# Optimization experiments

Measured on AMD Instinct MI355X. Metric: run time of the kernel, lower is better.

Reference implementation:

```python
import jax, jax.numpy as jnp
import numpy as np
from jax import lax

C_OUT, C_IN, KH, KW = 16, 16, 3, 3
STRIDE = (1, 1)
PADDING = ((1, 1), (1, 1))  # symmetric 'same' padding for 3x3, stride 1
DILATION = (1, 1)


def setup_inputs() -> dict:
    key = jax.random.key(0)
    kx, kw = jax.random.split(key)
    x = jax.random.normal(kx, (8, C_IN, 512, 512), dtype=jnp.float32)
    # Conv2DUF stores the conv weight flattened: [out_channels, in_channels*kh*kw]
    weight = jax.random.normal(kw, (C_OUT, C_IN * KH * KW), dtype=jnp.float32) * 0.1
    return {"x": x, "weight": weight}


def reference(x, weight):
    # forward(): F.conv2d(x, weight.reshape(original shape), stride/padding/dilation/groups)
    w = weight.reshape(C_OUT, C_IN, KH, KW)
    out = lax.conv_general_dilated(
        x, w,
        window_strides=STRIDE,
        padding=PADDING,
        rhs_dilation=DILATION,
        dimension_numbers=("NCHW", "OIHW", "NCHW"),
        feature_group_count=1,
    )
    return out  # [8, 16, 512, 512]
```

## Files before the change

### kernel.cpp

```cpp
#include <hip/hip_runtime.h>
#include <hip/hip_bf16.h>


#define IH 512
#define IW 512
#define CI 16
#define CO 16
#define TH 16
#define TW 32
#define LROWS (TH + 2)
#define LCOLS (TW + 2)
#define NITEMS (LROWS * (TW / 4) * 4)

typedef short short8  __attribute__((ext_vector_type(8)));
typedef short short4v __attribute__((ext_vector_type(4)));
typedef float f32x4   __attribute__((ext_vector_type(4)));

__device__ __forceinline__ short f32_to_bf16_bits(float v) {
    __hip_bfloat16 b = __float2bfloat16(v);
    return __builtin_bit_cast(short, b);
}

struct ItemInfo {
    const float* src;
    int pb;
    int ws;
    int cg;
    bool ok;
};

__device__ __forceinline__ ItemInfo item_info(int i, int hbase, int wbase,
                                              const float* __restrict__ xn) {
    ItemInfo t;
    t.ws = i & 7;
    t.cg = (i >> 3) & 3;
    const int row = i >> 5;
    const int gh  = hbase - 1 + row;
    t.ok  = (unsigned)gh < (unsigned)IH;
    t.src = xn + ((size_t)(t.cg * 4) * IH + gh) * IW + (wbase + 4 * t.ws);
    t.pb  = row * LCOLS + 1 + 4 * t.ws;
    return t;
}

__device__ __forceinline__ void item_load(const ItemInfo& t, f32x4 v[4]) {
    if (t.ok) {
#pragma unroll
        for (int jj = 0; jj < 4; ++jj)
            v[jj] = *(const f32x4*)(t.src + (size_t)jj * IH * IW);
    }
}

__device__ __forceinline__ void item_store(const ItemInfo& t, const f32x4 v[4],
                                           short* lds) {
    short4v pk[4];
    if (t.ok) {
#pragma unroll
        for (int j = 0; j < 4; ++j)
#pragma unroll
            for (int jj = 0; jj < 4; ++jj)
                pk[j][jj] = f32_to_bf16_bits(v[jj][j]);
    } else {
#pragma unroll
        for (int j = 0; j < 4; ++j) pk[j] = (short4v){0, 0, 0, 0};
    }
#pragma unroll
    for (int k = 0; k < 4; ++k) {
        const int j     = (k + t.ws) & 3;
        const int pixel = t.pb + j;
        const int slot  = t.cg ^ ((pixel >> 1) & 2);
        *(short4v*)&lds[pixel * 16 + slot * 4] = pk[j];
    }
}

__global__ __launch_bounds__(256, 6)
void conv3x3_mfma(const float* __restrict__ x, const float* __restrict__ wgt,
                  float* __restrict__ out) {
    __shared__ short lds[LROWS * LCOLS * CI];

    const int tid  = threadIdx.x;
    const int wave = tid >> 6;
    const int lane = tid & 63;
    const int quad = lane >> 4;
    const int l15  = lane & 15;

    const int bid   = blockIdx.x;
    const int n     = bid & 7;
    const int t     = bid >> 3;
    const int wbase = (t & 15) * TW;
    const int hbase = (t >> 4) * TH;

    const float* xn = x + (size_t)n * CI * IH * IW;

    ItemInfo t0 = item_info(tid,       hbase, wbase, xn);
    ItemInfo t1 = item_info(tid + 256, hbase, wbase, xn);
    f32x4 v0[4], v1[4];
    item_load(t0, v0);
    item_load(t1, v1);
    item_store(t0, v0, lds);
    const bool has2 = tid < (NITEMS - 512);
    ItemInfo t2 = item_info(has2 ? (tid + 512) : tid, hbase, wbase, xn);
    if (has2) item_load(t2, v0);
    item_store(t1, v1, lds);
    if (has2) item_store(t2, v0, lds);

    if (tid < 144) {
        const int cg4  = tid & 3;
        const int col2 = (tid >> 2) & 1;
        const int row  = tid >> 3;
        const int c    = col2 ? (LCOLS - 1) : 0;
        const int gh   = hbase - 1 + row;
        const int gw   = wbase - 1 + c;
        const bool ok  = ((unsigned)gh < (unsigned)IH) && ((unsigned)gw < (unsigned)IW);
        short4v pk;
#pragma unroll
        for (int j = 0; j < 4; ++j) {
            const float v = ok ? xn[((size_t)(cg4 * 4 + j) * IH + gh) * IW + gw] : 0.0f;
            pk[j] = f32_to_bf16_bits(v);
        }
        const int pixel = row * LCOLS + c;
        const int slot  = cg4 ^ ((pixel >> 1) & 2);
        *(short4v*)&lds[pixel * 16 + slot * 4] = pk;
    }

    short8 afrag[5];
#pragma unroll
    for (int f = 0; f < 5; ++f) {
#pragma unroll
        for (int j = 0; j < 8; ++j) {
            const int k = f * 32 + quad * 8 + j;
            float val = 0.0f;
            if (k < 144) {
                const int ci  = k & 15;
                const int tap = k >> 4;
                val = wgt[l15 * 144 + ci * 9 + tap];
            }
            afrag[f][j] = f32_to_bf16_bits(val);
        }
    }
    __syncthreads();

    const int q = quad & 1;
    int doff[5];
#pragma unroll
    for (int f = 0; f < 5; ++f) {
        const int tap = (f < 4) ? (f * 2 + (quad >> 1)) : 8;
        const int kh  = tap / 3;
        const int kw  = tap - kh * 3;
        doff[f] = kh * LCOLS + kw;
    }

    f32x4 acc[4][2];
#pragma unroll
    for (int r = 0; r < 4; ++r)
#pragma unroll
        for (int c4 = 0; c4 < 2; ++c4)
            acc[r][c4] = (f32x4){0.f, 0.f, 0.f, 0.f};

#pragma unroll
    for (int r = 0; r < 4; ++r) {
        const int hl = wave * 4 + r;
#pragma unroll
        for (int c4 = 0; c4 < 2; ++c4) {
            const int wl    = c4 * 16 + l15;
            const int pbase = hl * LCOLS + wl;
#pragma unroll
            for (int f = 0; f < 5; ++f) {
                const int pixel = pbase + doff[f];
                const int half  = q ^ ((pixel >> 2) & 1);
                const short8 b  = *(const short8*)&lds[pixel * 16 + half * 8];
                acc[r][c4] = __builtin_amdgcn_mfma_f32_16x16x32_bf16(afrag[f], b, acc[r][c4], 0, 0, 0);
            }
        }
    }

    float* on = out + (size_t)n * CO * IH * IW;
#pragma unroll
    for (int r = 0; r < 4; ++r) {
        const int gh = hbase + wave * 4 + r;
#pragma unroll
        for (int c4 = 0; c4 < 2; ++c4) {
            const int gw = wbase + c4 * 16 + l15;
#pragma unroll
            for (int reg = 0; reg < 4; ++reg) {
                const int co = quad * 4 + reg;
                on[((size_t)co * IH + gh) * IW + gw] = acc[r][c4][reg];
            }
        }
    }
}

extern "C" void kernel_launch(void* const* d_in, const int* in_sizes, int n_in,
                              void* d_out, int out_size, void* d_ws, size_t ws_size,
                              hipStream_t stream) {
    const float* x = (const float*)d_in[0];
    const float* w = (const float*)d_in[1];
    float* out     = (float*)d_out;

    dim3 grid((IW / TW) * (IH / TH) * 8);
    dim3 block(256);
    conv3x3_mfma<<<grid, block, 0, stream>>>(x, w, out);
}
```

Measured before the change: 290.2 us.

## Pre-transpose input to NHWC bf16 in workspace and stage tiles via direct global-to-LDS loads

Adds a prep kernel that converts the NCHW fp32 input into a channel-interleaved NHWC bf16 workspace, with swizzled halves, and pre-packs the weights into bf16 MFMA fragments. The conv kernel then fills its LDS halo tile with global_load_lds 16-byte loads, using a zero page for out-of-bounds pixels, and reads weight fragments from global memory. The goal is cheaper, coalesced staging and less conversion work inside the conv kernel. In exchange it adds an extra kernel launch plus a full read of the fp32 input and a write and re-read of a bf16 copy, which increases total memory traffic. The old fused kernel is kept as a fallback when the workspace is too small.

```diff
diff --git a/kernel.cpp b/kernel.cpp
--- a/kernel.cpp
+++ b/kernel.cpp
@@ -10,22 +10,195 @@
 #define TW 32
 #define LROWS (TH + 2)
 #define LCOLS (TW + 2)
-#define NITEMS (LROWS * (TW / 4) * 4)
+#define ROWB  (LCOLS * CI * 2)
+#define NCHUNK (LROWS * LCOLS * 2)
+
+#define XT_OFF   0
+#define XT_BYTES ((size_t)8 * IH * IW * CI * 2)
+#define ZP_OFF   XT_BYTES
+#define ZP_BYTES 4096
+#define WPK_OFF  (XT_BYTES + ZP_BYTES)
+#define WPK_BYTES 5120
+#define WS_NEED  (WPK_OFF + (size_t)WPK_BYTES)
 
 typedef short short8  __attribute__((ext_vector_type(8)));
 typedef short short4v __attribute__((ext_vector_type(4)));
 typedef float f32x4   __attribute__((ext_vector_type(4)));
+typedef unsigned int uint4v __attribute__((ext_vector_type(4)));
 
 __device__ __forceinline__ short f32_to_bf16_bits(float v) {
     __hip_bfloat16 b = __float2bfloat16(v);
     return __builtin_bit_cast(short, b);
 }
 
+__device__ __forceinline__ void gload_lds16(const void* g, void* l) {
+    __builtin_amdgcn_global_load_lds(
+        (const __attribute__((address_space(1))) void*)g,
+        (__attribute__((address_space(3))) void*)l, 16, 0, 0);
+}
+
+__global__ __launch_bounds__(256, 4)
+void conv_prep(const float* __restrict__ x, const float* __restrict__ wgt,
+               char* __restrict__ ws) {
+    short* xt    = (short*)(ws + XT_OFF);
+    char*  zpage = ws + ZP_OFF;
+    short* wpk   = (short*)(ws + WPK_OFF);
+
+    const int tid = threadIdx.x;
+    const int p   = blockIdx.x * 256 + tid;
+    const int n   = p >> 16;
+    const int rem = p & 65535;
+    const int h   = rem >> 7;
+    const int wq  = rem & 127;
+    const int w0  = wq * 4;
+    const int s   = wq & 1;
+
+    const float* src = x + (size_t)n * CI * IH * IW + (size_t)h * IW + w0;
+    f32x4 v[16];
+#pragma unroll
+    for (int c = 0; c < 16; ++c)
+        v[c] = *(const f32x4*)(src + (size_t)c * IH * IW);
+
+    short* dst = xt + ((size_t)(n * IH + h) * IW + w0) * CI;
+#pragma unroll
+    for (int jj = 0; jj < 4; ++jj) {
+        unsigned int dl[8];
+#pragma unroll
+        for (int k = 0; k < 8; ++k) {
+            const unsigned lo = (unsigned short)f32_to_bf16_bits(v[2 * k][jj]);
+            const unsigned hi = (unsigned short)f32_to_bf16_bits(v[2 * k + 1][jj]);
+            dl[k] = lo | (hi << 16);
+        }
+        uint4v A = {dl[0], dl[1], dl[2], dl[3]};
+        uint4v B = {dl[4], dl[5], dl[6], dl[7]};
+        uint4v first  = s ? B : A;
+        uint4v second = s ? A : B;
+        uint4v* o = (uint4v*)(dst + (size_t)jj * CI);
+        o[0] = first;
+        o[1] = second;
+    }
+
+    if (blockIdx.x == 0) {
+        *(uint4v*)(zpage + tid * 16) = (uint4v){0, 0, 0, 0};
+#pragma unroll
+        for (int i = 0; i < 10; ++i) {
+            const int e  = i * 256 + tid;
+            const int co = e & 15;
+            const int k  = e >> 4;
+            float val = 0.0f;
+            if (k < 144) {
+                const int ci  = k & 15;
+                const int tap = k >> 4;
+                val = wgt[co * 144 + ci * 9 + tap];
+            }
+            wpk[co * 160 + k] = f32_to_bf16_bits(val);
+        }
+    }
+}
+
+__global__ __launch_bounds__(256, 8)
+void conv3x3_lds(const char* __restrict__ ws, float* __restrict__ out) {
+    __shared__ short lds[LROWS * LCOLS * CI];
+
+    const short* xt    = (const short*)(ws + XT_OFF);
+    const char*  zpage = ws + ZP_OFF;
+    const short* wpk   = (const short*)(ws + WPK_OFF);
+
+    const int tid  = threadIdx.x;
+    const int wave = tid >> 6;
+    const int lane = tid & 63;
+    const int quad = lane >> 4;
+    const int l15  = lane & 15;
+
+    const int bid   = blockIdx.x;
+    const int n     = bid & 7;
+    const int t     = bid >> 3;
+    const int wbase = (t & 15) * TW;
+    const int hbase = (t >> 4) * TH;
+
+#pragma unroll
+    for (int it = 0; it < 4; ++it) {
+        const int c   = it * 256 + tid;
+        const int row = c / 68;
+        const int o   = c - row * 68;
+        const int gh  = hbase - 1 + row;
+        const int gw  = wbase - 1 + (o >> 1);
+        const bool ok = ((unsigned)gh < (unsigned)IH) && ((unsigned)gw < (unsigned)IW);
+        const char* g = ok
+            ? (const char*)(xt + (((size_t)(n * IH + gh) * IW + gw) * CI + (o & 1) * 8))
+            : zpage;
+        char* l = (char*)lds + (size_t)(it * 256 + wave * 64) * 16;
+        gload_lds16(g, l);
+    }
+    if (tid < 200) {
+        const int c   = 1024 + tid;
+        const int row = c / 68;
+        const int o   = c - row * 68;
+        const int gh  = hbase - 1 + row;
+        const int gw  = wbase - 1 + (o >> 1);
+        const bool ok = ((unsigned)gh < (unsigned)IH) && ((unsigned)gw < (unsigned)IW);
+        const char* g = ok
+            ? (const char*)(xt + (((size_t)(n * IH + gh) * IW + gw) * CI + (o & 1) * 8))
+            : zpage;
+        const uint4v v = *(const uint4v*)g;
+        *(uint4v*)((char*)lds + (size_t)c * 16) = v;
+    }
+
+    const int q = quad & 1;
+    int kh_[5], kw_[5];
+#pragma unroll
+    for (int f = 0; f < 5; ++f) {
+        const int tap = (f < 4) ? (f * 2 + (quad >> 1)) : 8;
+        kh_[f] = tap / 3;
+        kw_[f] = tap - (tap / 3) * 3;
+    }
+
+    __syncthreads();
+
+    f32x4 acc[4][2];
+#pragma unroll
+    for (int r = 0; r < 4; ++r)
+#pragma unroll
+        for (int c4 = 0; c4 < 2; ++c4)
+            acc[r][c4] = (f32x4){0.f, 0.f, 0.f, 0.f};
+
+    const short* wp = wpk + l15 * 160 + quad * 8;
+#pragma unroll
+    for (int f = 0; f < 5; ++f) {
+        const short8 afrag = *(const short8*)(wp + f * 32);
+#pragma unroll
+        for (int r = 0; r < 4; ++r) {
+            const int row = wave * 4 + r + kh_[f];
+#pragma unroll
+            for (int c4 = 0; c4 < 2; ++c4) {
+                const int col = c4 * 16 + l15 + kw_[f];
+                const int s   = ((col + 31) >> 2) & 1;
+                const int m   = q ^ s;
+                const short8 b = *(const short8*)&lds[row * (LCOLS * CI) + col * CI + m * 8];
+                acc[r][c4] = __builtin_amdgcn_mfma_f32_16x16x32_bf16(afrag, b, acc[r][c4], 0, 0, 0);
+            }
+        }
+    }
+
+    float* on = out + (size_t)n * CO * IH * IW;
+#pragma unroll
+    for (int r = 0; r < 4; ++r) {
+        const int gh = hbase + wave * 4 + r;
+#pragma unroll
+        for (int c4 = 0; c4 < 2; ++c4) {
+            const int gw = wbase + c4 * 16 + l15;
+#pragma unroll
+            for (int reg = 0; reg < 4; ++reg) {
+                const int co = quad * 4 + reg;
+                on[((size_t)co * IH + gh) * IW + gw] = acc[r][c4][reg];
+            }
+        }
+    }
+}
+
 struct ItemInfo {
     const float* src;
-    int pb;
-    int ws;
-    int cg;
+    int pb, ws, cg;
     bool ok;
 };
 
@@ -73,8 +246,8 @@
 }
 
 __global__ __launch_bounds__(256, 6)
-void conv3x3_mfma(const float* __restrict__ x, const float* __restrict__ wgt,
-                  float* __restrict__ out) {
+void conv3x3_mfma_fb(const float* __restrict__ x, const float* __restrict__ wgt,
+                     float* __restrict__ out) {
     __shared__ short lds[LROWS * LCOLS * CI];
 
     const int tid  = threadIdx.x;
@@ -97,7 +270,7 @@
     item_load(t0, v0);
     item_load(t1, v1);
     item_store(t0, v0, lds);
-    const bool has2 = tid < (NITEMS - 512);
+    const bool has2 = tid < (LROWS * (TW / 4) * 4 - 512);
     ItemInfo t2 = item_info(has2 ? (tid + 512) : tid, hbase, wbase, xn);
     if (has2) item_load(t2, v0);
     item_store(t1, v1, lds);
@@ -196,7 +369,13 @@
     const float* w = (const float*)d_in[1];
     float* out     = (float*)d_out;
 
-    dim3 grid((IW / TW) * (IH / TH) * 8);
-    dim3 block(256);
-    conv3x3_mfma<<<grid, block, 0, stream>>>(x, w, out);
-}
+    if (ws_size >= WS_NEED) {
+        dim3 gprep(2048);
+        conv_prep<<<gprep, dim3(256), 0, stream>>>(x, w, (char*)d_ws);
+        dim3 gconv((IW / TW) * (IH / TH) * 8);
+        conv3x3_lds<<<gconv, dim3(256), 0, stream>>>((const char*)d_ws, out);
+    } else {
+        dim3 grid((IW / TW) * (IH / TH) * 8);
+        conv3x3_mfma_fb<<<grid, dim3(256), 0, stream>>>(x, w, out);
+    }
+}
```

Result: slower. 298.5 us (+2.9%).

## Widen conv tile to 64 columns and hoist all global loads ahead of LDS stores

Applied to the files above, without the earlier changes.

Doubles the output tile width so each block covers 16x64 pixels, cutting the halo overhead per output and halving the number of blocks. The staging code now issues all four main input loads plus the halo loads before any LDS writes, and interleaves the weight fragment conversion between stores so more memory latency is hidden. Register use and LDS footprint grow, so launch bounds are lowered to 4 blocks per CU, which reduces occupancy and the number of resident waves.

```diff
diff --git a/kernel.cpp b/kernel.cpp
--- a/kernel.cpp
+++ b/kernel.cpp
@@ -7,7 +7,7 @@
 #define CI 16
 #define CO 16
 #define TH 16
-#define TW 32
+#define TW 64
 #define LROWS (TH + 2)
 #define LCOLS (TW + 2)
 #define NITEMS (LROWS * (TW / 4) * 4)
@@ -32,9 +32,9 @@
 __device__ __forceinline__ ItemInfo item_info(int i, int hbase, int wbase,
                                               const float* __restrict__ xn) {
     ItemInfo t;
-    t.ws = i & 7;
-    t.cg = (i >> 3) & 3;
-    const int row = i >> 5;
+    t.ws = i & 15;
+    t.cg = (i >> 4) & 3;
+    const int row = i >> 6;
     const int gh  = hbase - 1 + row;
     t.ok  = (unsigned)gh < (unsigned)IH;
     t.src = xn + ((size_t)(t.cg * 4) * IH + gh) * IW + (wbase + 4 * t.ws);
@@ -72,7 +72,7 @@
     }
 }
 
-__global__ __launch_bounds__(256, 6)
+__global__ __launch_bounds__(256, 4)
 void conv3x3_mfma(const float* __restrict__ x, const float* __restrict__ wgt,
                   float* __restrict__ out) {
     __shared__ short lds[LROWS * LCOLS * CI];
@@ -86,24 +86,25 @@
     const int bid   = blockIdx.x;
     const int n     = bid & 7;
     const int t     = bid >> 3;
-    const int wbase = (t & 15) * TW;
-    const int hbase = (t >> 4) * TH;
+    const int wbase = (t & 7) * TW;
+    const int hbase = (t >> 3) * TH;
 
     const float* xn = x + (size_t)n * CI * IH * IW;
 
     ItemInfo t0 = item_info(tid,       hbase, wbase, xn);
     ItemInfo t1 = item_info(tid + 256, hbase, wbase, xn);
-    f32x4 v0[4], v1[4];
+    ItemInfo t2 = item_info(tid + 512, hbase, wbase, xn);
+    ItemInfo t3 = item_info(tid + 768, hbase, wbase, xn);
+    f32x4 v0[4], v1[4], v2[4], v3[4];
     item_load(t0, v0);
     item_load(t1, v1);
-    item_store(t0, v0, lds);
-    const bool has2 = tid < (NITEMS - 512);
-    ItemInfo t2 = item_info(has2 ? (tid + 512) : tid, hbase, wbase, xn);
-    if (has2) item_load(t2, v0);
-    item_store(t1, v1, lds);
-    if (has2) item_store(t2, v0, lds);
-
-    if (tid < 144) {
+    item_load(t2, v2);
+    item_load(t3, v3);
+
+    const bool halo = tid < 144;
+    float hv0 = 0.f, hv1 = 0.f, hv2 = 0.f, hv3 = 0.f;
+    int hpix = 0, hslot = 0;
+    if (halo) {
         const int cg4  = tid & 3;
         const int col2 = (tid >> 2) & 1;
         const int row  = tid >> 3;
@@ -111,16 +112,22 @@
         const int gh   = hbase - 1 + row;
         const int gw   = wbase - 1 + c;
         const bool ok  = ((unsigned)gh < (unsigned)IH) && ((unsigned)gw < (unsigned)IW);
-        short4v pk;
-#pragma unroll
-        for (int j = 0; j < 4; ++j) {
-            const float v = ok ? xn[((size_t)(cg4 * 4 + j) * IH + gh) * IW + gw] : 0.0f;
-            pk[j] = f32_to_bf16_bits(v);
-        }
-        const int pixel = row * LCOLS + c;
-        const int slot  = cg4 ^ ((pixel >> 1) & 2);
-        *(short4v*)&lds[pixel * 16 + slot * 4] = pk;
-    }
+        if (ok) {
+            const float* hs = xn + ((size_t)(cg4 * 4) * IH + gh) * IW + gw;
+            hv0 = hs[0];
+            hv1 = hs[(size_t)IH * IW];
+            hv2 = hs[(size_t)2 * IH * IW];
+            hv3 = hs[(size_t)3 * IH * IW];
+        }
+        hpix  = row * LCOLS + c;
+        hslot = cg4 ^ ((hpix >> 1) & 2);
+    }
+
+    item_store(t0, v0, lds);
+
+    const bool act4 = tid < (NITEMS - 1024);
+    ItemInfo t4 = item_info(act4 ? (1024 + tid) : tid, hbase, wbase, xn);
+    if (act4) item_load(t4, v0);
 
     short8 afrag[5];
 #pragma unroll
@@ -137,6 +144,19 @@
             afrag[f][j] = f32_to_bf16_bits(val);
         }
     }
+
+    item_store(t1, v1, lds);
+    item_store(t2, v2, lds);
+    item_store(t3, v3, lds);
+    if (act4) item_store(t4, v0, lds);
+    if (halo) {
+        short4v pk;
+        pk[0] = f32_to_bf16_bits(hv0);
+        pk[1] = f32_to_bf16_bits(hv1);
+        pk[2] = f32_to_bf16_bits(hv2);
+        pk[3] = f32_to_bf16_bits(hv3);
+        *(short4v*)&lds[hpix * 16 + hslot * 4] = pk;
+    }
     __syncthreads();
 
     const int q = quad & 1;
@@ -149,18 +169,18 @@
         doff[f] = kh * LCOLS + kw;
     }
 
-    f32x4 acc[4][2];
+    f32x4 acc[4][4];
 #pragma unroll
     for (int r = 0; r < 4; ++r)
 #pragma unroll
-        for (int c4 = 0; c4 < 2; ++c4)
+        for (int c4 = 0; c4 < 4; ++c4)
             acc[r][c4] = (f32x4){0.f, 0.f, 0.f, 0.f};
 
 #pragma unroll
     for (int r = 0; r < 4; ++r) {
         const int hl = wave * 4 + r;
 #pragma unroll
-        for (int c4 = 0; c4 < 2; ++c4) {
+        for (int c4 = 0; c4 < 4; ++c4) {
             const int wl    = c4 * 16 + l15;
             const int pbase = hl * LCOLS + wl;
 #pragma unroll
@@ -178,7 +198,7 @@
     for (int r = 0; r < 4; ++r) {
         const int gh = hbase + wave * 4 + r;
 #pragma unroll
-        for (int c4 = 0; c4 < 2; ++c4) {
+        for (int c4 = 0; c4 < 4; ++c4) {
             const int gw = wbase + c4 * 16 + l15;
 #pragma unroll
             for (int reg = 0; reg < 4; ++reg) {
```

New measurement: 296.6 us. 1.02x slower.
